# Kernel optimization log

Measured on AMD Instinct MI355X. Metric: run time of the kernel, lower is better.

Reference implementation:

```python
import jax, jax.numpy as jnp
import numpy as np

K = 4          # neighbors
R = 2          # step_ratio
OUT = 64       # output_size

def knn_idx(x, k):
    # x: (B, C, N) -> indices of k nearest neighbors (incl. self): (B, N, k)
    xx = jnp.sum(x * x, axis=1)                       # (B, N)
    inner = jnp.einsum('bcn,bcm->bnm', x, x)          # (B, N, N)
    neg_dist = 2.0 * inner - xx[:, :, None] - xx[:, None, :]
    _, idx = jax.lax.top_k(neg_dist, k)               # largest neg_dist = nearest
    return idx

def setup_inputs() -> dict:
    key = jax.random.key(0)
    ks = jax.random.split(key, 7)
    B, C, N = 16, 64, 2048
    s = 0.05
    return {
        'x':  jax.random.normal(ks[0], (B, C, N), jnp.float32),
        'w1': jax.random.normal(ks[1], (OUT, 2 * C), jnp.float32) * s,
        'b1': jax.random.normal(ks[2], (OUT,), jnp.float32) * s,
        'w2': jax.random.normal(ks[3], (OUT * R, 2 * C + OUT), jnp.float32) * s,
        'b2': jax.random.normal(ks[4], (OUT * R,), jnp.float32) * s,
        'w3': jax.random.normal(ks[5], (OUT, OUT), jnp.float32) * s,
        'b3': jax.random.normal(ks[6], (OUT,), jnp.float32) * s,
    }

def reference(x, w1, b1, w2, b2, w3, b3):
    B, C, N = x.shape
    idx = knn_idx(x, K)                                # (B, N, K)
    xt = jnp.transpose(x, (0, 2, 1))                   # (B, N, C)
    neighbors = xt[jnp.arange(B)[:, None, None], idx]  # (B, N, K, C)
    center = jnp.broadcast_to(xt[:, :, None, :], neighbors.shape)
    feat = jnp.concatenate([center, neighbors], axis=-1)   # (B, N, K, 2C), minus_center=False
    # get_graph_feature returns (B, 2C, N, K); module permutes to (B, 2C, K, N)
    f = jnp.transpose(feat, (0, 3, 2, 1))              # (B, 2C, K, N)
    e1 = jnp.einsum('oc,bckn->bokn', w1, f) + b1[None, :, None, None]
    e = jax.nn.relu(jnp.concatenate([e1, f], axis=1))  # (B, 2C+OUT, K, N)
    e2 = jax.nn.relu(jnp.einsum('oc,bckn->bokn', w2, e) + b2[None, :, None, None])  # (B, OUT*R, K, N)
    # permute(0,2,3,1) -> (B,K,N,OUT*R), view -> (B,K,N*R,OUT), permute -> (B,OUT,K,N*R)
    e2 = jnp.transpose(e2, (0, 2, 3, 1)).reshape(B, K, N * R, OUT)
    e2 = jnp.transpose(e2, (0, 3, 1, 2))               # (B, OUT, K, N*R)
    e3 = jnp.einsum('oc,bckn->bokn', w3, e2) + b3[None, :, None, None]
    return jnp.max(e3, axis=2)                          # (B, OUT, N*R)
```

## Files before the change

### kernel.cpp

```cpp
#include <hip/hip_runtime.h>
#include <hip/hip_bf16.h>

#define BB 16
#define CC 64
#define NN 2048
#define KK 4
#define NPART 4
#define JPER (NN / NPART)
#define NCAND 32
#define RSTRIDE 80

typedef unsigned short u16;
typedef unsigned int u32;
typedef __attribute__((ext_vector_type(4))) float f32x4;
typedef __attribute__((ext_vector_type(16))) float f32x16;
typedef __attribute__((ext_vector_type(8))) short short8;

__device__ __forceinline__ float bf2f(u16 u) {
    unsigned int x = ((unsigned int)u) << 16;
    float f;
    __builtin_memcpy(&f, &x, 4);
    return f;
}
__device__ __forceinline__ u16 f2bf(float f) {
    __hip_bfloat16 h = __float2bfloat16(f);
    u16 u;
    __builtin_memcpy(&u, &h, 2);
    return u;
}
__device__ __forceinline__ unsigned int pk2(float a, float b) {
    return (unsigned int)f2bf(a) | ((unsigned int)f2bf(b) << 16);
}
__device__ __forceinline__ u32 umx(u32 a, u32 b) { return a > b ? a : b; }
__device__ __forceinline__ u32 umn(u32 a, u32 b) { return a < b ? a : b; }

__global__ __launch_bounds__(256) void k_prep(const float* __restrict__ x,
                                              float* __restrict__ xt,
                                              u16* __restrict__ xpk) {
    int b = blockIdx.y;
    int n = blockIdx.x * 256 + threadIdx.x;
    const float* xb = x + (size_t)b * CC * NN;
    float v[CC];
    float s = 0.f;
#pragma unroll
    for (int c = 0; c < CC; c++) {
        v[c] = xb[(size_t)c * NN + n];
        s = fmaf(v[c], v[c], s);
    }
    float4* dst = (float4*)(xt + ((size_t)b * NN + n) * CC);
#pragma unroll
    for (int q = 0; q < 16; q++) {
        dst[q] = make_float4(v[4 * q], v[4 * q + 1], v[4 * q + 2], v[4 * q + 3]);
    }
    u16* dp = xpk + ((size_t)b * NN + n) * RSTRIDE;
#pragma unroll
    for (int q = 0; q < 8; q++) {
        uint4 u;
        u.x = pk2(v[8 * q], v[8 * q + 1]);
        u.y = pk2(v[8 * q + 2], v[8 * q + 3]);
        u.z = pk2(v[8 * q + 4], v[8 * q + 5]);
        u.w = pk2(v[8 * q + 6], v[8 * q + 7]);
        *(uint4*)(dp + q * 8) = u;
    }
    u16 hi = f2bf(s);
    u16 lo = f2bf(s - bf2f(hi));
    uint4 u8;
    u8.x = (unsigned int)hi | ((unsigned int)lo << 16);
    u8.y = 0x00003F80u;
    u8.z = 0; u8.w = 0;
    *(uint4*)(dp + 64) = u8;
    uint4 z = {0, 0, 0, 0};
    *(uint4*)(dp + 72) = z;
}

__global__ __launch_bounds__(256) void k_wprep(const float* __restrict__ w1,
                                               const float* __restrict__ w2,
                                               const float* __restrict__ w3,
                                               u16* __restrict__ wb1,
                                               u16* __restrict__ wb2,
                                               u16* __restrict__ wb3) {
    int t = blockIdx.x * 256 + threadIdx.x;
    int stride = gridDim.x * 256;
    for (int idx = t; idx < 64 * 128; idx += stride) {
        int o = idx >> 7, k = idx & 127;
        int cb = o >> 4, lr = o & 15, ks = k >> 5, g = (k >> 3) & 3, e = k & 7;
        wb1[((cb * 4 + ks) * 64 + g * 16 + lr) * 8 + e] = f2bf(w1[idx]);
    }
    for (int idx = t; idx < 128 * 192; idx += stride) {
        int o = idx / 192, k = idx - o * 192;
        int cb = o >> 4, lr = o & 15, ks = k >> 5, g = (k >> 3) & 3, e = k & 7;
        wb2[((cb * 6 + ks) * 64 + g * 16 + lr) * 8 + e] = f2bf(w2[idx]);
    }
    for (int idx = t; idx < 64 * 64; idx += stride) {
        int o = idx >> 6, k = idx & 63;
        int cb = o >> 4, lr = o & 15, ks = k >> 5, g = (k >> 3) & 3, e = k & 7;
        wb3[((cb * 2 + ks) * 64 + g * 16 + lr) * 8 + e] = f2bf(w3[idx]);
    }
}

__global__ __launch_bounds__(256) void k_knn3(const u16* __restrict__ xpk,
                                              u16* __restrict__ cand) {
    int ib = blockIdx.x;
    int part = blockIdx.y;
    int b = blockIdx.z;
    int tid = threadIdx.x;
    int i0 = ib * 128;
    int j00 = part * JPER;

    __shared__ u16 Bb[2 * 2 * 10 * 32 * 8];

    int w = tid >> 6, l = tid & 63;
    int lc = l & 31, lh = l >> 5;
    int hb4 = lh * 4;

    short8 ifrag[5];
    {
        const u16* ip = xpk + ((size_t)b * NN + i0 + w * 32 + lc) * RSTRIDE + lh * 8;
#pragma unroll
        for (int ks = 0; ks < 4; ks++) ifrag[ks] = *(const short8*)(ip + ks * 16);
        short8 f4 = {0, 0, 0, 0, 0, 0, 0, 0};
        if (lh == 0) {
            f4[0] = (short)0xBF00;
            f4[1] = (short)0xBF00;
            f4[2] = (short)0x4300;
        }
        ifrag[4] = f4;
    }

    u32 v0 = 0, v1 = 0, v2 = 0, v3 = 0;

#define CE(a, b) { u32 mx_ = umx(a, b); b = umn(a, b); a = mx_; }

#define STAGE(rr, bf)                                                              \
    {                                                                              \
        int jb = j00 + (rr) * 64;                                                  \
        for (int g = tid; g < 640; g += 256) {                                     \
            int rw = g / 10, c = g - rw * 10;                                      \
            uint4 u = *(const uint4*)(xpk + ((size_t)b * NN + jb + rw) * RSTRIDE + \
                                      c * 8);                                      \
            int sub = rw >> 5, r32 = rw & 31;                                      \
            *(uint4*)((char*)Bb + (bf) * 10240 + sub * 5120 + c * 512 +            \
                      ((r32 ^ (c & 7)) * 16)) = u;                                 \
        }                                                                          \
    }

    STAGE(0, 0);

    for (int r = 0; r < JPER / 64; r++) {
        __syncthreads();
        if (r + 1 < JPER / 64) STAGE(r + 1, (r + 1) & 1);

        const char* bufp = (const char*)Bb + (r & 1) * 10240;
        f32x16 acc0, acc1;
#pragma unroll
        for (int e = 0; e < 16; e++) {
            acc0[e] = 0.f;
            acc1[e] = 0.f;
        }
#pragma unroll
        for (int ks = 0; ks < 5; ks++) {
            int c = ks * 2 + lh;
            int boff = c * 512 + ((lc ^ (c & 7)) * 16);
            short8 a0 = *(const short8*)(bufp + boff);
            short8 a1 = *(const short8*)(bufp + 5120 + boff);
            acc0 = __builtin_amdgcn_mfma_f32_32x32x16_bf16(a0, ifrag[ks], acc0, 0, 0, 0);
            acc1 = __builtin_amdgcn_mfma_f32_32x32x16_bf16(a1, ifrag[ks], acc1, 0, 0, 0);
        }
#pragma unroll
        for (int sub = 0; sub < 2; sub++) {
            const f32x16& acc = sub ? acc1 : acc0;
            int jlb = r * 64 + sub * 32 + hb4;
            u32 kk[16];
#pragma unroll
            for (int rg = 0; rg < 16; rg++) {
                u32 u;
                float f = acc[rg];
                __builtin_memcpy(&u, &f, 4);
                int coff = (rg & 3) + 8 * (rg >> 2);
                kk[rg] = (u & ~0x1FFu) | (u32)(jlb + coff);
            }
#pragma unroll
            for (int q = 0; q < 4; q++) {
                int p = q * 4;
                CE(kk[p + 0], kk[p + 2]); CE(kk[p + 1], kk[p + 3]);
                CE(kk[p + 0], kk[p + 1]); CE(kk[p + 2], kk[p + 3]);
                CE(kk[p + 1], kk[p + 2]);
            }
            kk[0] = umx(kk[0], kk[7]); kk[1] = umx(kk[1], kk[6]);
            kk[2] = umx(kk[2], kk[5]); kk[3] = umx(kk[3], kk[4]);
            CE(kk[0], kk[2]); CE(kk[1], kk[3]); CE(kk[0], kk[1]); CE(kk[2], kk[3]);
            kk[8] = umx(kk[8], kk[15]); kk[9] = umx(kk[9], kk[14]);
            kk[10] = umx(kk[10], kk[13]); kk[11] = umx(kk[11], kk[12]);
            CE(kk[8], kk[10]); CE(kk[9], kk[11]); CE(kk[8], kk[9]); CE(kk[10], kk[11]);
            kk[0] = umx(kk[0], kk[11]); kk[1] = umx(kk[1], kk[10]);
            kk[2] = umx(kk[2], kk[9]); kk[3] = umx(kk[3], kk[8]);
            CE(kk[0], kk[2]); CE(kk[1], kk[3]); CE(kk[0], kk[1]); CE(kk[2], kk[3]);
            v0 = umx(v0, kk[3]); v1 = umx(v1, kk[2]);
            v2 = umx(v2, kk[1]); v3 = umx(v3, kk[0]);
            CE(v0, v2); CE(v1, v3); CE(v0, v1); CE(v2, v3);
        }
    }
#undef STAGE
#undef CE

    size_t cb = ((size_t)b * NN + i0 + w * 32 + lc) * NCAND + part * 8 + lh * 4;
    cand[cb + 0] = (u16)(j00 + (v0 & 0x1FF));
    cand[cb + 1] = (u16)(j00 + (v1 & 0x1FF));
    cand[cb + 2] = (u16)(j00 + (v2 & 0x1FF));
    cand[cb + 3] = (u16)(j00 + (v3 & 0x1FF));
}

__global__ __launch_bounds__(256) void k_knn_merge(const float* __restrict__ xt,
                                                   const u16* __restrict__ cand,
                                                   int* __restrict__ nidx) {
    __shared__ double sv[8 * 33];
    __shared__ int si[8 * 33];

    int tid = threadIdx.x;
    int pl = tid >> 5;
    int c = tid & 31;
    size_t gp = (size_t)blockIdx.x * 8 + pl;
    int b = (int)(gp >> 11);

    int j = cand[gp * NCAND + c];
    const float4* xi = (const float4*)(xt + gp * CC);
    const float4* xj = (const float4*)(xt + (((size_t)b << 11) + j) * CC);

    double d0 = 0.0, d1 = 0.0, s0 = 0.0, s1 = 0.0;
#pragma unroll
    for (int q = 0; q < 16; q += 2) {
        float4 a0 = xi[q], a1 = xi[q + 1];
        float4 c0 = xj[q], c1 = xj[q + 1];
        d0 += (double)a0.x * c0.x + (double)a0.y * c0.y +
              (double)a0.z * c0.z + (double)a0.w * c0.w;
        s0 += (double)c0.x * c0.x + (double)c0.y * c0.y +
              (double)c0.z * c0.z + (double)c0.w * c0.w;
        d1 += (double)a1.x * c1.x + (double)a1.y * c1.y +
              (double)a1.z * c1.z + (double)a1.w * c1.w;
        s1 += (double)c1.x * c1.x + (double)c1.y * c1.y +
              (double)c1.z * c1.z + (double)c1.w * c1.w;
    }
    sv[pl * 33 + c] = 2.0 * (d0 + d1) - (s0 + s1);
    si[pl * 33 + c] = j;
    __syncthreads();

    if (tid < 8) {
        int p = tid;
        double v4[4];
        int id4[4];
#pragma unroll
        for (int s = 0; s < 4; s++) {
            v4[s] = -1e300;
            id4[s] = 0x7fffffff;
        }
        for (int cc = 0; cc < NCAND; cc++) {
            double cv = sv[p * 33 + cc];
            int ci = si[p * 33 + cc];
#pragma unroll
            for (int s = 0; s < 4; s++) {
                bool take = (cv > v4[s]) || (cv == v4[s] && ci < id4[s]);
                double nv = take ? cv : v4[s];
                int ni = take ? ci : id4[s];
                double ov = take ? v4[s] : cv;
                int oi = take ? id4[s] : ci;
                v4[s] = nv;
                id4[s] = ni;
                cv = ov;
                ci = oi;
            }
        }
        size_t gp2 = (size_t)blockIdx.x * 8 + p;
#pragma unroll
        for (int s = 0; s < 4; s++) nidx[gp2 * 4 + s] = id4[s];
    }
}

__global__ __launch_bounds__(256) void k_mlp(const u16* __restrict__ xpk,
                                             const int* __restrict__ nidx,
                                             const u16* __restrict__ wb1,
                                             const u16* __restrict__ wb2,
                                             const u16* __restrict__ wb3,
                                             const float* __restrict__ b1,
                                             const float* __restrict__ b2,
                                             const float* __restrict__ b3,
                                             float* __restrict__ out) {
    int nch = blockIdx.x;
    int b = blockIdx.y;
    int n0 = nch * 16;
    int tid = threadIdx.x;

    __shared__ u16 Fb[64 * 128];
    __shared__ u16 E1b[64 * 64];
    __shared__ u16 E2b[64 * 128];
    __shared__ float Ob[64 * 36];
    __shared__ int ji[64];

    if (tid < 64) ji[tid] = nidx[((size_t)b * NN + n0) * KK + tid];
    __syncthreads();

    for (int g = tid; g < 64 * 16; g += 256) {
        int it = g >> 4, q = g & 15;
        int half = q >> 3, cq = q & 7;
        int srcn = half ? ji[it] : (n0 + (it >> 2));
        uint4 u = *(const uint4*)(xpk + ((size_t)b * NN + srcn) * RSTRIDE + cq * 8);
        int byte = (it * 256 + half * 128 + cq * 16) ^ ((it & 7) << 4);
        *(uint4*)((char*)Fb + byte) = u;
    }
    __syncthreads();

    int w = tid >> 6, l = tid & 63;
    int lr = l & 15, lg = l >> 4;

    {
        f32x4 acc[4];
#pragma unroll
        for (int g = 0; g < 4; g++) acc[g] = (f32x4){0.f, 0.f, 0.f, 0.f};
#pragma unroll
        for (int ks = 0; ks < 4; ks++) {
            short8 bw = *(const short8*)(wb1 + ((size_t)(w * 4 + ks) * 64 + l) * 8);
#pragma unroll
            for (int g = 0; g < 4; g++) {
                int arow = g * 16 + lr;
                int off = (arow * 256 + ks * 64 + lg * 16) ^ ((arow & 7) << 4);
                short8 a = *(const short8*)((const char*)Fb + off);
                acc[g] = __builtin_amdgcn_mfma_f32_16x16x32_bf16(a, bw, acc[g], 0, 0, 0);
            }
        }
        float bias = b1[w * 16 + lr];
#pragma unroll
        for (int g = 0; g < 4; g++) {
#pragma unroll
            for (int q = 0; q < 4; q++) {
                int item = g * 16 + lg * 4 + q;
                float vv = fmaxf(acc[g][q] + bias, 0.f);
                int byte = (item * 128 + (w * 16 + lr) * 2) ^ ((item & 7) << 4);
                *(u16*)((char*)E1b + byte) = f2bf(vv);
            }
        }
    }
    __syncthreads();

    {
        f32x4 acc[4][2];
#pragma unroll
        for (int g = 0; g < 4; g++)
#pragma unroll
            for (int c2 = 0; c2 < 2; c2++) acc[g][c2] = (f32x4){0.f, 0.f, 0.f, 0.f};
#pragma unroll
        for (int ks = 0; ks < 6; ks++) {
            short8 bw0 = *(const short8*)(wb2 + ((size_t)((w * 2) * 6 + ks) * 64 + l) * 8);
            short8 bw1 = *(const short8*)(wb2 + ((size_t)((w * 2 + 1) * 6 + ks) * 64 + l) * 8);
#pragma unroll
            for (int g = 0; g < 4; g++) {
                int arow = g * 16 + lr;
                int aswz = (arow & 7) << 4;
                short8 a;
                if (ks < 2) {
                    int off = (arow * 128 + ks * 64 + lg * 16) ^ aswz;
                    a = *(const short8*)((const char*)E1b + off);
                } else {
                    int off = (arow * 256 + (ks - 2) * 64 + lg * 16) ^ aswz;
                    uint4 u = *(const uint4*)((const char*)Fb + off);
                    unsigned int m;
                    m = ((u.x >> 15) & 0x10001u) * 0xFFFFu; u.x &= ~m;
                    m = ((u.y >> 15) & 0x10001u) * 0xFFFFu; u.y &= ~m;
                    m = ((u.z >> 15) & 0x10001u) * 0xFFFFu; u.z &= ~m;
                    m = ((u.w >> 15) & 0x10001u) * 0xFFFFu; u.w &= ~m;
                    __builtin_memcpy(&a, &u, 16);
                }
                acc[g][0] = __builtin_amdgcn_mfma_f32_16x16x32_bf16(a, bw0, acc[g][0], 0, 0, 0);
                acc[g][1] = __builtin_amdgcn_mfma_f32_16x16x32_bf16(a, bw1, acc[g][1], 0, 0, 0);
            }
        }
#pragma unroll
        for (int c2 = 0; c2 < 2; c2++) {
            float bias = b2[(w * 2 + c2) * 16 + lr];
#pragma unroll
            for (int g = 0; g < 4; g++) {
#pragma unroll
                for (int q = 0; q < 4; q++) {
                    int item = g * 16 + lg * 4 + q;
                    float vv = fmaxf(acc[g][c2][q] + bias, 0.f);
                    int byte = (item * 256 + ((w * 2 + c2) * 16 + lr) * 2) ^ ((item & 7) << 4);
                    *(u16*)((char*)E2b + byte) = f2bf(vv);
                }
            }
        }
    }
    __syncthreads();

    {
        f32x4 acc[4][2];
#pragma unroll
        for (int g = 0; g < 4; g++)
#pragma unroll
            for (int r = 0; r < 2; r++) acc[g][r] = (f32x4){0.f, 0.f, 0.f, 0.f};
#pragma unroll
        for (int ks = 0; ks < 2; ks++) {
            short8 bw = *(const short8*)(wb3 + ((size_t)(w * 2 + ks) * 64 + l) * 8);
#pragma unroll
            for (int g = 0; g < 4; g++) {
                int arow = g * 16 + lr;
                int aswz = (arow & 7) << 4;
#pragma unroll
                for (int r = 0; r < 2; r++) {
                    int off = (arow * 256 + r * 128 + ks * 64 + lg * 16) ^ aswz;
                    short8 a = *(const short8*)((const char*)E2b + off);
                    acc[g][r] = __builtin_amdgcn_mfma_f32_16x16x32_bf16(a, bw, acc[g][r], 0, 0, 0);
                }
            }
        }
        float bias = b3[w * 16 + lr];
        int o = w * 16 + lr;
#pragma unroll
        for (int g = 0; g < 4; g++) {
            int nl = g * 4 + lg;
#pragma unroll
            for (int r = 0; r < 2; r++) {
                float m = fmaxf(fmaxf(acc[g][r][0], acc[g][r][1]),
                                fmaxf(acc[g][r][2], acc[g][r][3])) + bias;
                Ob[o * 36 + nl * 2 + r] = m;
            }
        }
    }
    __syncthreads();

    {
        int o = tid >> 2, q = tid & 3;
        float4 v0 = *(const float4*)&Ob[o * 36 + q * 8];
        float4 v1 = *(const float4*)&Ob[o * 36 + q * 8 + 4];
        float* dst = out + ((size_t)(b * 64 + o)) * 4096 + n0 * 2 + q * 8;
        ((float4*)dst)[0] = v0;
        ((float4*)dst)[1] = v1;
    }
}

extern "C" void kernel_launch(void* const* d_in, const int* in_sizes, int n_in,
                              void* d_out, int out_size, void* d_ws, size_t ws_size,
                              hipStream_t stream) {
    const float* x = (const float*)d_in[0];
    const float* w1 = (const float*)d_in[1];
    const float* b1 = (const float*)d_in[2];
    const float* w2 = (const float*)d_in[3];
    const float* b2 = (const float*)d_in[4];
    const float* w3 = (const float*)d_in[5];
    const float* b3 = (const float*)d_in[6];
    float* out = (float*)d_out;

    float* xt = (float*)d_ws;
    u16* xpk = (u16*)(xt + (size_t)BB * NN * CC);
    int* nidx = (int*)(xpk + (size_t)BB * NN * RSTRIDE);
    u16* cand = (u16*)(nidx + (size_t)BB * NN * KK);
    u16* wb1 = cand + (size_t)BB * NN * NCAND;
    u16* wb2 = wb1 + 64 * 128;
    u16* wb3 = wb2 + 128 * 192;

    k_prep<<<dim3(NN / 256, BB), 256, 0, stream>>>(x, xt, xpk);
    k_wprep<<<dim3(32), 256, 0, stream>>>(w1, w2, w3, wb1, wb2, wb3);
    k_knn3<<<dim3(NN / 128, NPART, BB), 256, 0, stream>>>(xpk, cand);
    k_knn_merge<<<dim3(BB * NN / 8), 256, 0, stream>>>(xt, cand, nidx);
    k_mlp<<<dim3(NN / 16, BB), 256, 0, stream>>>(xpk, nidx, wb1, wb2, wb3, b1, b2, b3, out);
}
```

Before: 119.5 us.

## Precompute fp64 squared norms and split merge dot products across 16 lanes

The prep kernel now computes each point's double-precision squared norm once and stores it, so the candidate re-ranking kernel no longer recomputes the neighbour norm for every candidate. The merge kernel is restructured so 16 lanes cooperate on one query point, each loading a float4 slice of the candidate row. Partial dot products are combined with xor shuffles, giving coalesced loads instead of one thread streaming a whole 256-byte row. Each block now handles 16 points, which adds shuffle and loop overhead plus an extra fp64 workspace array.

New measurement: 113.5 us. -5.0%, faster.

```diff
diff --git a/kernel.cpp b/kernel.cpp
--- a/kernel.cpp
+++ b/kernel.cpp
@@ -36,22 +36,26 @@
 
 __global__ __launch_bounds__(256) void k_prep(const float* __restrict__ x,
                                               float* __restrict__ xt,
+                                              double* __restrict__ xx64,
                                               u16* __restrict__ xpk) {
     int b = blockIdx.y;
     int n = blockIdx.x * 256 + threadIdx.x;
     const float* xb = x + (size_t)b * CC * NN;
     float v[CC];
     float s = 0.f;
+    double s64 = 0.0;
 #pragma unroll
     for (int c = 0; c < CC; c++) {
         v[c] = xb[(size_t)c * NN + n];
         s = fmaf(v[c], v[c], s);
+        s64 += (double)v[c] * (double)v[c];
     }
     float4* dst = (float4*)(xt + ((size_t)b * NN + n) * CC);
 #pragma unroll
     for (int q = 0; q < 16; q++) {
         dst[q] = make_float4(v[4 * q], v[4 * q + 1], v[4 * q + 2], v[4 * q + 3]);
     }
+    xx64[b * NN + n] = s64;
     u16* dp = xpk + ((size_t)b * NN + n) * RSTRIDE;
 #pragma unroll
     for (int q = 0; q < 8; q++) {
@@ -211,40 +215,41 @@
 }
 
 __global__ __launch_bounds__(256) void k_knn_merge(const float* __restrict__ xt,
+                                                   const double* __restrict__ xx64,
                                                    const u16* __restrict__ cand,
                                                    int* __restrict__ nidx) {
-    __shared__ double sv[8 * 33];
-    __shared__ int si[8 * 33];
+    __shared__ double sv[16 * 33];
+    __shared__ u16 ji[16 * 33];
 
     int tid = threadIdx.x;
-    int pl = tid >> 5;
-    int c = tid & 31;
-    size_t gp = (size_t)blockIdx.x * 8 + pl;
-    int b = (int)(gp >> 11);
-
-    int j = cand[gp * NCAND + c];
-    const float4* xi = (const float4*)(xt + gp * CC);
-    const float4* xj = (const float4*)(xt + (((size_t)b << 11) + j) * CC);
-
-    double d0 = 0.0, d1 = 0.0, s0 = 0.0, s1 = 0.0;
-#pragma unroll
-    for (int q = 0; q < 16; q += 2) {
-        float4 a0 = xi[q], a1 = xi[q + 1];
-        float4 c0 = xj[q], c1 = xj[q + 1];
-        d0 += (double)a0.x * c0.x + (double)a0.y * c0.y +
-              (double)a0.z * c0.z + (double)a0.w * c0.w;
-        s0 += (double)c0.x * c0.x + (double)c0.y * c0.y +
-              (double)c0.z * c0.z + (double)c0.w * c0.w;
-        d1 += (double)a1.x * c1.x + (double)a1.y * c1.y +
-              (double)a1.z * c1.z + (double)a1.w * c1.w;
-        s1 += (double)c1.x * c1.x + (double)c1.y * c1.y +
-              (double)c1.z * c1.z + (double)c1.w * c1.w;
-    }
-    sv[pl * 33 + c] = 2.0 * (d0 + d1) - (s0 + s1);
-    si[pl * 33 + c] = j;
-    __syncthreads();
-
-    if (tid < 8) {
+    int g = tid >> 4;
+    int q = tid & 15;
+    size_t gp0 = (size_t)blockIdx.x * 16;
+    size_t bbase = (gp0 >> 11) << 11;
+
+    for (int idx = tid; idx < 16 * 32; idx += 256) {
+        int p = idx >> 5, c = idx & 31;
+        ji[p * 33 + c] = cand[(gp0 + p) * NCAND + c];
+    }
+    __syncthreads();
+
+    float4 a = ((const float4*)(xt + (gp0 + g) * CC))[q];
+
+#pragma unroll 4
+    for (int c = 0; c < NCAND; c++) {
+        int j = ji[g * 33 + c];
+        float4 bv = ((const float4*)(xt + (bbase + j) * CC))[q];
+        double d = (double)a.x * (double)bv.x + (double)a.y * (double)bv.y +
+                   (double)a.z * (double)bv.z + (double)a.w * (double)bv.w;
+        d += __shfl_xor(d, 8);
+        d += __shfl_xor(d, 4);
+        d += __shfl_xor(d, 2);
+        d += __shfl_xor(d, 1);
+        if (q == 0) sv[g * 33 + c] = 2.0 * d - xx64[bbase + j];
+    }
+    __syncthreads();
+
+    if (tid < 16) {
         int p = tid;
         double v4[4];
         int id4[4];
@@ -255,7 +260,7 @@
         }
         for (int cc = 0; cc < NCAND; cc++) {
             double cv = sv[p * 33 + cc];
-            int ci = si[p * 33 + cc];
+            int ci = ji[p * 33 + cc];
 #pragma unroll
             for (int s = 0; s < 4; s++) {
                 bool take = (cv > v4[s]) || (cv == v4[s] && ci < id4[s]);
@@ -269,7 +274,7 @@
                 ci = oi;
             }
         }
-        size_t gp2 = (size_t)blockIdx.x * 8 + p;
+        size_t gp2 = gp0 + p;
 #pragma unroll
         for (int s = 0; s < 4; s++) nidx[gp2 * 4 + s] = id4[s];
     }
@@ -449,15 +454,16 @@
 
     float* xt = (float*)d_ws;
     u16* xpk = (u16*)(xt + (size_t)BB * NN * CC);
-    int* nidx = (int*)(xpk + (size_t)BB * NN * RSTRIDE);
+    double* xx64 = (double*)(xpk + (size_t)BB * NN * RSTRIDE);
+    int* nidx = (int*)(xx64 + (size_t)BB * NN);
     u16* cand = (u16*)(nidx + (size_t)BB * NN * KK);
     u16* wb1 = cand + (size_t)BB * NN * NCAND;
     u16* wb2 = wb1 + 64 * 128;
     u16* wb3 = wb2 + 128 * 192;
 
-    k_prep<<<dim3(NN / 256, BB), 256, 0, stream>>>(x, xt, xpk);
+    k_prep<<<dim3(NN / 256, BB), 256, 0, stream>>>(x, xt, xx64, xpk);
     k_wprep<<<dim3(32), 256, 0, stream>>>(w1, w2, w3, wb1, wb2, wb3);
     k_knn3<<<dim3(NN / 128, NPART, BB), 256, 0, stream>>>(xpk, cand);
-    k_knn_merge<<<dim3(BB * NN / 8), 256, 0, stream>>>(xt, cand, nidx);
+    k_knn_merge<<<dim3(BB * NN / 16), 256, 0, stream>>>(xt, xx64, cand, nidx);
     k_mlp<<<dim3(NN / 16, BB), 256, 0, stream>>>(xpk, nidx, wb1, wb2, wb3, b1, b2, b3, out);
 }
```
